# Kernel tuning notes

Measured on AMD Instinct MI355X. Metric: run time of the kernel, lower is better.

## Reference

```python
import jax, jax.numpy as jnp
import numpy as np
import math

B, N, D, H, BS = 1, 2048, 1024, 16, 256  # batch, seq, d_model, heads, block_size


def setup_inputs() -> dict:
    key = jax.random.key(0)
    ks = jax.random.split(key, 8)
    s = 0.02  # init scale for projection weights
    return {
        "x": jax.random.normal(ks[0], (B, N, D), jnp.float32),
        "distance_bias": jax.random.uniform(ks[1], (N, N), dtype=jnp.float32),
        "Wq": jax.random.normal(ks[2], (D, D), jnp.float32) * s,
        "bq": jnp.zeros((D,), jnp.float32),
        "Wk": jax.random.normal(ks[3], (D, D), jnp.float32) * s,
        "bk": jnp.zeros((D,), jnp.float32),
        "Wv": jax.random.normal(ks[4], (D, D), jnp.float32) * s,
        "bv": jnp.zeros((D,), jnp.float32),
        "Wo": jax.random.normal(ks[5], (D, D), jnp.float32) * s,
        "bo": jnp.zeros((D,), jnp.float32),
    }


def reference(x, distance_bias, Wq, bq, Wk, bk, Wv, bv, Wo, bo):
    Bm, Nm, Dm = x.shape
    dk = Dm // H
    scale = 1.0 / math.sqrt(dk)
    nb = Nm // BS  # number of blocks along sequence

    def proj(W, b):
        # torch Linear: x @ W.T + b, then split heads -> [B, H, N, dk]
        return (x @ W.T + b).reshape(Bm, Nm, H, dk).transpose(0, 2, 1, 3)

    Q, K, V = proj(Wq, bq), proj(Wk, bk), proj(Wv, bv)

    # scores with toroidal bias subtracted (matches `scores - bias_block`)
    scores = jnp.einsum('bhqd,bhkd->bhqk', Q, K) * scale - distance_bias[None, None]
    # view as [B, H, n_qblk, BS, n_kblk, BS] and softmax PER (q-block, k-block)
    s6 = scores.reshape(Bm, H, nb, BS, nb, BS)
    w = jax.nn.softmax(s6, axis=-1)  # softmax over keys within each kv block

    Vb = V.reshape(Bm, H, nb, BS, dk)
    # sum over all kv blocks of (per-block softmax) @ V_block
    num = jnp.einsum('bhqsnk,bhnkd->bhqsd', w, Vb)  # [B,H,nb,BS,dk]
    # accumulated normalizer = sum of per-block softmax weights over all kv blocks
    norm = jnp.sum(w, axis=(4, 5))  # [B,H,nb,BS]
    O = num / (norm[..., None] + 1e-8)

    O = O.reshape(Bm, H, Nm, dk).transpose(0, 2, 1, 3).reshape(Bm, Nm, Dm)
    return O @ Wo.T + bo
```

## Files before the change

### kernel.cpp

```cpp
#include <hip/hip_runtime.h>
#include <hip/hip_fp16.h>

typedef _Float16 half8 __attribute__((ext_vector_type(8)));
typedef _Float16 half4v __attribute__((ext_vector_type(4)));
typedef float f32x4 __attribute__((ext_vector_type(4)));

#define NSEQ 2048
#define DMOD 1024
#define NHEAD 16
#define DK 64

#define GLOAD_LDS16(gp, lp) __builtin_amdgcn_global_load_lds(                 \
    (const __attribute__((address_space(1))) void*)(gp),                      \
    (__attribute__((address_space(3))) void*)(lp), 16, 0, 0)

#define WAIT_VM(n) (0xF70 | (n))


__global__ __launch_bounds__(256) void cast_pack(
    const float* __restrict__ x, const float* __restrict__ wq,
    const float* __restrict__ wk, const float* __restrict__ wv,
    const float* __restrict__ wo, _Float16* __restrict__ dst)
{
    const int w = blockIdx.x * 4 + (threadIdx.x >> 6);
    const int ln = threadIdx.x & 63, m = ln & 15, qd = ln >> 4;
    const float* src; _Float16* d; int loc;
    if (w < 4096) { src = x; d = dst; loc = w; }
    else {
        const int w2 = w - 4096, mat = w2 >> 11;
        loc = w2 & 2047;
        src = mat == 0 ? wq : mat == 1 ? wk : mat == 2 ? wv : wo;
        d = dst + 2097152 + mat * 1048576;
    }
    const int st = loc >> 5, kc = loc & 31;
    const float* p = src + (size_t)(st * 16 + m) * 1024 + kc * 32 + qd * 8;
    float4 a = *(const float4*)p, b = *(const float4*)(p + 4);
    half8 h;
    h[0] = (_Float16)a.x; h[1] = (_Float16)a.y; h[2] = (_Float16)a.z; h[3] = (_Float16)a.w;
    h[4] = (_Float16)b.x; h[5] = (_Float16)b.y; h[6] = (_Float16)b.z; h[7] = (_Float16)b.w;
    *(half8*)(d + (size_t)(loc * 64 + ln) * 8) = h;
}

__global__ __launch_bounds__(256) void cvt_bias(
    const float* __restrict__ src, _Float16* __restrict__ dst)
{
    int i = (blockIdx.x * 256 + threadIdx.x) * 4;
    float4 v = *(const float4*)(src + i);
    half4v h;
    h[0] = (_Float16)v.x; h[1] = (_Float16)v.y;
    h[2] = (_Float16)v.z; h[3] = (_Float16)v.w;
    *(half4v*)(dst + i) = h;
}

__global__ __launch_bounds__(256) void combine(
    const _Float16* __restrict__ a, const _Float16* __restrict__ b,
    _Float16* __restrict__ o)
{
    int i = (blockIdx.x * 256 + threadIdx.x) * 8;
    half8 x = *(const half8*)(a + i);
    half8 y = *(const half8*)(b + i);
    half8 r;
#pragma unroll
    for (int j = 0; j < 8; ++j) r[j] = (_Float16)((float)x[j] + (float)y[j]);
    *(half8*)(o + i) = r;
}

template<int BM, int BN, int MODE>
__global__ __launch_bounds__(256) void tgemm(
    const _Float16* __restrict__ A,
    const _Float16* __restrict__ W0, const _Float16* __restrict__ W1,
    const _Float16* __restrict__ W2,
    const float* __restrict__ b0, const float* __restrict__ b1,
    const float* __restrict__ b2,
    _Float16* __restrict__ oQ, _Float16* __restrict__ oK,
    _Float16* __restrict__ oV, float* __restrict__ oF)
{
    constexpr int MT = BM / 32, NT = BN / 32;
    constexpr int NA = BM / 64, NB = BN / 64;
    __shared__ _Float16 sA[3 * BM * 32];
    __shared__ _Float16 sB[3 * BN * 32];
    const int tid = threadIdx.x, wv = tid >> 6, ln = tid & 63;
    const int m = ln & 15, qd = ln >> 4;
    const int row0 = blockIdx.x * BM;

    int sel = 0, colbase;
    const _Float16* W; const float* bias;
    if constexpr (MODE == 0) {
        sel = blockIdx.y >> 3;
        colbase = (blockIdx.y & 7) * BN;
        W = sel == 0 ? W0 : sel == 1 ? W1 : W2;
        bias = sel == 0 ? b0 : sel == 1 ? b1 : b2;
    } else {
        colbase = blockIdx.y * BN;
        W = W0; bias = b0;
    }
    const int wr = wv >> 1, wc = wv & 1;

    f32x4 acc[MT][NT];
#pragma unroll
    for (int i = 0; i < MT; ++i)
#pragma unroll
        for (int j = 0; j < NT; ++j) acc[i][j] = (f32x4){0.f, 0.f, 0.f, 0.f};

    auto stage = [&](int kc, int b) {
        _Float16* dA = sA + b * (BM * 32);
        _Float16* dB = sB + b * (BN * 32);
#pragma unroll
        for (int ra = 0; ra < NA; ++ra) {
            const int st = ra * 4 + wv;
            GLOAD_LDS16(A + ((size_t)((row0 >> 4) + st) * 32 + kc) * 512 + ln * 8,
                        dA + st * 512);
        }
#pragma unroll
        for (int rb = 0; rb < NB; ++rb) {
            const int st = rb * 4 + wv;
            GLOAD_LDS16(W + ((size_t)((colbase >> 4) + st) * 32 + kc) * 512 + ln * 8,
                        dB + st * 512);
        }
    };
    auto step = [&](int b) {
        const _Float16* cA = sA + b * (BM * 32);
        const _Float16* cB = sB + b * (BN * 32);
        half8 af[MT], bf[NT];
#pragma unroll
        for (int i = 0; i < MT; ++i)
            af[i] = *(const half8*)(cA + ((wr * MT + i) * 64 + ln) * 8);
#pragma unroll
        for (int j = 0; j < NT; ++j)
            bf[j] = *(const half8*)(cB + ((wc * NT + j) * 64 + ln) * 8);
#pragma unroll
        for (int i = 0; i < MT; ++i)
#pragma unroll
            for (int j = 0; j < NT; ++j)
                acc[i][j] = __builtin_amdgcn_mfma_f32_16x16x32_f16(af[i], bf[j], acc[i][j], 0, 0, 0);
    };

    stage(0, 0);
    stage(1, 1);
#pragma unroll
    for (int kc = 0; kc < 31; ++kc) {
        __builtin_amdgcn_s_waitcnt(WAIT_VM(NA + NB));
        __builtin_amdgcn_s_barrier();
        if (kc < 30) stage(kc + 2, (kc + 2) % 3);
        step(kc % 3);
    }
    __builtin_amdgcn_s_waitcnt(WAIT_VM(0));
    __builtin_amdgcn_s_barrier();
    step(1);

#pragma unroll
    for (int j = 0; j < NT; ++j) {
        const int col = colbase + wc * (BN / 2) + j * 16 + m;
        const float bv = bias[col];
#pragma unroll
        for (int i = 0; i < MT; ++i) {
            const int crow0 = row0 + wr * (BM / 2) + i * 16 + qd * 4;
            if constexpr (MODE == 1) {
#pragma unroll
                for (int r = 0; r < 4; ++r)
                    oF[(size_t)(crow0 + r) * DMOD + col] = acc[i][j][r] + bv;
            } else {
                const int h = col >> 6, d = col & 63;
                if (sel == 0) {
#pragma unroll
                    for (int r = 0; r < 4; ++r)
                        oQ[h * (NSEQ * DK) + (crow0 + r) * DK + d] =
                            (_Float16)((acc[i][j][r] + bv) * 0.125f);
                } else if (sel == 1) {
#pragma unroll
                    for (int r = 0; r < 4; ++r) {
                        const int n = crow0 + r;
                        oK[(size_t)(((h * 16 + (n >> 7)) * 16
                                     + ((n >> 4) & 7) * 2 + (d >> 5)) * 64
                                    + (n & 15) + 16 * ((d >> 3) & 3)) * 8
                           + (d & 7)] = (_Float16)(acc[i][j][r] + bv);
                    }
                } else {
                    half4v hv;
#pragma unroll
                    for (int r = 0; r < 4; ++r) hv[r] = (_Float16)(acc[i][j][r] + bv);
                    const int n0 = crow0;
                    *(half4v*)(oV + (size_t)(((h * 16 + (n0 >> 7)) * 16
                                              + ((n0 >> 5) & 3) * 4 + ((d >> 4) & 3)) * 64
                                             + (d & 15) + 16 * ((n0 >> 3) & 3)) * 8
                               + (n0 & 7)) = hv;
                }
            }
        }
    }
}

__global__ __launch_bounds__(256, 2) void attn(
    const _Float16* __restrict__ Q, const _Float16* __restrict__ Kt,
    const _Float16* __restrict__ Vt, const _Float16* __restrict__ bias_h,
    _Float16* __restrict__ Op)
{
    __shared__ _Float16 sK[8192];
    __shared__ _Float16 sV[8192];
    __shared__ _Float16 sP[16384];
    const int tid = threadIdx.x, wv = tid >> 6, ln = tid & 63;
    const int m = ln & 15, qd = ln >> 4;
    const int h = blockIdx.x;
    const int q0w = blockIdx.y * 128 + wv * 32;
    const int kvb = blockIdx.z * 8;
    const _Float16* Qh = Q + h * (NSEQ * DK);
    const _Float16* Kh = Kt + h * (NSEQ * DK) + kvb * 8192;
    const _Float16* Vh = Vt + h * (NSEQ * DK) + kvb * 8192;
    const _Float16* brow0 = bias_h + (size_t)(q0w + m) * NSEQ + kvb * 128;
    const _Float16* brow1 = bias_h + (size_t)(q0w + 16 + m) * NSEQ + kvb * 128;

    half8 qf[2][2];
#pragma unroll
    for (int u = 0; u < 2; ++u) {
        qf[u][0] = *(const half8*)(Qh + (q0w + u * 16 + m) * DK + qd * 8);
        qf[u][1] = *(const half8*)(Qh + (q0w + u * 16 + m) * DK + 32 + qd * 8);
    }

    f32x4 oacc[2][4], oU[2][4];
#pragma unroll
    for (int u = 0; u < 2; ++u)
#pragma unroll
        for (int v = 0; v < 4; ++v) {
            oacc[u][v] = (f32x4){0.f, 0.f, 0.f, 0.f};
            oU[u][v]   = (f32x4){0.f, 0.f, 0.f, 0.f};
        }
    float bsum[2] = {0.f, 0.f};

    for (int ls = 0; ls < 8; ++ls) {
        if (ls) __syncthreads();
#pragma unroll
        for (int j = 0; j < 4; ++j) {
            const int f = j * 4 + wv;
            GLOAD_LDS16(Kh + ls * 8192 + f * 512 + ln * 8, sK + f * 512);
            GLOAD_LDS16(Vh + ls * 8192 + f * 512 + ln * 8, sV + f * 512);
        }
        half4v bcur[2][8];
#pragma unroll
        for (int t = 0; t < 8; ++t) {
            bcur[0][t] = *(const half4v*)(brow0 + ls * 128 + t * 16 + qd * 4);
            bcur[1][t] = *(const half4v*)(brow1 + ls * 128 + t * 16 + qd * 4);
        }
        __syncthreads();

#pragma unroll
        for (int t = 0; t < 8; ++t) {
            half8 kf0 = *(const half8*)(sK + ((t * 2 + 0) * 64 + ln) * 8);
            half8 kf1 = *(const half8*)(sK + ((t * 2 + 1) * 64 + ln) * 8);
#pragma unroll
            for (int u = 0; u < 2; ++u) {
                f32x4 s = {0.f, 0.f, 0.f, 0.f};
                s = __builtin_amdgcn_mfma_f32_16x16x32_f16(kf0, qf[u][0], s, 0, 0, 0);
                s = __builtin_amdgcn_mfma_f32_16x16x32_f16(kf1, qf[u][1], s, 0, 0, 0);
                float p0 = __expf(s[0] - (float)bcur[u][t][0]);
                float p1 = __expf(s[1] - (float)bcur[u][t][1]);
                float p2 = __expf(s[2] - (float)bcur[u][t][2]);
                float p3 = __expf(s[3] - (float)bcur[u][t][3]);
                bsum[u] += (p0 + p1) + (p2 + p3);
                half4v ph;
                ph[0] = (_Float16)p0; ph[1] = (_Float16)p1;
                ph[2] = (_Float16)p2; ph[3] = (_Float16)p3;
                *(half4v*)(sP + wv * 4096 + u * 2048 + (t >> 1) * 512
                           + (((t & 1) * 2 + (qd >> 1)) * 16 + m) * 8
                           + (qd & 1) * 4) = ph;
            }
        }

#pragma unroll
        for (int kk = 0; kk < 4; ++kk) {
            half8 pa0 = *(const half8*)(sP + wv * 4096 + kk * 512 + ln * 8);
            half8 pa1 = *(const half8*)(sP + wv * 4096 + 2048 + kk * 512 + ln * 8);
#pragma unroll
            for (int vt = 0; vt < 4; ++vt) {
                half8 vb = *(const half8*)(sV + ((kk * 4 + vt) * 64 + ln) * 8);
                oU[0][vt] = __builtin_amdgcn_mfma_f32_16x16x32_f16(pa0, vb, oU[0][vt], 0, 0, 0);
                oU[1][vt] = __builtin_amdgcn_mfma_f32_16x16x32_f16(pa1, vb, oU[1][vt], 0, 0, 0);
            }
        }

        if (ls & 1) {
#pragma unroll
            for (int u = 0; u < 2; ++u) {
                float s2 = bsum[u];
                s2 += __shfl_xor(s2, 16, 64);
                s2 += __shfl_xor(s2, 32, 64);
                float inv = 1.0f / (8.0f * s2);
                float iv[4];
#pragma unroll
                for (int r = 0; r < 4; ++r) iv[r] = __shfl(inv, qd * 4 + r, 64);
#pragma unroll
                for (int vt = 0; vt < 4; ++vt) {
#pragma unroll
                    for (int r = 0; r < 4; ++r) oacc[u][vt][r] += iv[r] * oU[u][vt][r];
                    oU[u][vt] = (f32x4){0.f, 0.f, 0.f, 0.f};
                }
                bsum[u] = 0.f;
            }
        }
    }

    _Float16* Opz = Op + (size_t)blockIdx.z * 2097152;
#pragma unroll
    for (int u = 0; u < 2; ++u) {
        const int st = (q0w >> 4) + u;
#pragma unroll
        for (int vt = 0; vt < 4; ++vt) {
            const int d = h * 64 + vt * 16 + m;
            _Float16* base = Opz + (size_t)(st * 32 + (d >> 5)) * 512
                             + ((d >> 3) & 3) * 128 + (d & 7);
#pragma unroll
            for (int r = 0; r < 4; ++r)
                base[(qd * 4 + r) * 8] = (_Float16)oacc[u][vt][r];
        }
    }
}

extern "C" void kernel_launch(void* const* d_in, const int* in_sizes, int n_in,
                              void* d_out, int out_size, void* d_ws, size_t ws_size,
                              hipStream_t stream)
{
    const float* x  = (const float*)d_in[0];
    const float* db = (const float*)d_in[1];
    const float* Wq = (const float*)d_in[2];
    const float* bq = (const float*)d_in[3];
    const float* Wk = (const float*)d_in[4];
    const float* bk = (const float*)d_in[5];
    const float* Wv = (const float*)d_in[6];
    const float* bv = (const float*)d_in[7];
    const float* Wo = (const float*)d_in[8];
    const float* bo = (const float*)d_in[9];
    float* out = (float*)d_out;

    _Float16* ws  = (_Float16*)d_ws;
    _Float16* xh  = ws;
    _Float16* wqh = xh  + 2097152;
    _Float16* wkh = wqh + 1048576;
    _Float16* wvh = wkh + 1048576;
    _Float16* woh = wvh + 1048576;
    _Float16* Qb  = woh + 1048576;
    _Float16* Kb  = Qb  + 2097152;
    _Float16* Vtb = Kb  + 2097152;
    _Float16* Oh0 = Vtb + 2097152;
    _Float16* Oh1 = Oh0 + 2097152;
    _Float16* bh  = ws;

    cast_pack<<<3072, 256, 0, stream>>>(x, Wq, Wk, Wv, Wo, xh);

    tgemm<128, 128, 0><<<dim3(16, 24), 256, 0, stream>>>(
        xh, wqh, wkh, wvh, bq, bk, bv, Qb, Kb, Vtb, nullptr);

    cvt_bias<<<4096, 256, 0, stream>>>(db, bh);

    attn<<<dim3(NHEAD, NSEQ / 128, 2), 256, 0, stream>>>(Qb, Kb, Vtb, bh, Oh0);

    combine<<<1024, 256, 0, stream>>>(Oh0, Oh1, Oh0);

    tgemm<64, 128, 1><<<dim3(32, 8), 256, 0, stream>>>(
        Oh0, woh, nullptr, nullptr, bo, nullptr, nullptr,
        nullptr, nullptr, nullptr, out);
}
```

Before: 187.0 us.

## Double-buffer K tiles and prefetch next bias rows in attention loop

The attention kernel now double-buffers K tiles in LDS, issuing the next step's K loads while the current step computes. It also prefetches the next step's bias registers after the QK/softmax phase. Manual s_waitcnt counters and raw s_barrier calls replace __syncthreads, so V loads can keep flying during the score computation. The cost is an extra 16 KB of LDS, which may hurt the 2-blocks-per-CU occupancy. The hand-counted vmcnt values are also fragile and could cause races if they are wrong.

```diff
diff --git a/kernel.cpp b/kernel.cpp
--- a/kernel.cpp
+++ b/kernel.cpp
@@ -15,6 +15,9 @@
     (__attribute__((address_space(3))) void*)(lp), 16, 0, 0)
 
 #define WAIT_VM(n) (0xF70 | (n))
+#define WAIT_VM_BIG(n) ((((n) >> 4) << 14) | 0xF70 | ((n) & 0xF))
+
+template<bool B> struct Bc { static constexpr bool value = B; };
 
 
 __global__ __launch_bounds__(256) void cast_pack(
@@ -195,7 +198,7 @@
     const _Float16* __restrict__ Vt, const _Float16* __restrict__ bias_h,
     _Float16* __restrict__ Op)
 {
-    __shared__ _Float16 sK[8192];
+    __shared__ _Float16 sK[2][8192];
     __shared__ _Float16 sV[8192];
     __shared__ _Float16 sP[16384];
     const int tid = threadIdx.x, wv = tid >> 6, ln = tid & 63;
@@ -216,6 +219,18 @@
         qf[u][1] = *(const half8*)(Qh + (q0w + u * 16 + m) * DK + 32 + qd * 8);
     }
 
+#pragma unroll
+    for (int j = 0; j < 4; ++j) {
+        const int f = j * 4 + wv;
+        GLOAD_LDS16(Kh + f * 512 + ln * 8, sK[0] + f * 512);
+    }
+    half4v bcur[2][8];
+#pragma unroll
+    for (int t = 0; t < 8; ++t) {
+        bcur[0][t] = *(const half4v*)(brow0 + t * 16 + qd * 4);
+        bcur[1][t] = *(const half4v*)(brow1 + t * 16 + qd * 4);
+    }
+
     f32x4 oacc[2][4], oU[2][4];
 #pragma unroll
     for (int u = 0; u < 2; ++u)
@@ -226,26 +241,32 @@
         }
     float bsum[2] = {0.f, 0.f};
 
-    for (int ls = 0; ls < 8; ++ls) {
-        if (ls) __syncthreads();
+    auto do_step = [&](int ls, auto fc, auto lc) {
+        constexpr bool FIRST = decltype(fc)::value;
+        constexpr bool LAST  = decltype(lc)::value;
+        if constexpr (!FIRST) __builtin_amdgcn_s_barrier();
 #pragma unroll
         for (int j = 0; j < 4; ++j) {
             const int f = j * 4 + wv;
-            GLOAD_LDS16(Kh + ls * 8192 + f * 512 + ln * 8, sK + f * 512);
             GLOAD_LDS16(Vh + ls * 8192 + f * 512 + ln * 8, sV + f * 512);
         }
-        half4v bcur[2][8];
+        if constexpr (!LAST) {
+#pragma unroll
+            for (int j = 0; j < 4; ++j) {
+                const int f = j * 4 + wv;
+                GLOAD_LDS16(Kh + (ls + 1) * 8192 + f * 512 + ln * 8,
+                            sK[(ls + 1) & 1] + f * 512);
+            }
+        }
+        if constexpr (LAST) __builtin_amdgcn_s_waitcnt(WAIT_VM(4));
+        else                __builtin_amdgcn_s_waitcnt(WAIT_VM(8));
+        __builtin_amdgcn_s_barrier();
+
+        const _Float16* sKc = sK[ls & 1];
 #pragma unroll
         for (int t = 0; t < 8; ++t) {
-            bcur[0][t] = *(const half4v*)(brow0 + ls * 128 + t * 16 + qd * 4);
-            bcur[1][t] = *(const half4v*)(brow1 + ls * 128 + t * 16 + qd * 4);
-        }
-        __syncthreads();
-
-#pragma unroll
-        for (int t = 0; t < 8; ++t) {
-            half8 kf0 = *(const half8*)(sK + ((t * 2 + 0) * 64 + ln) * 8);
-            half8 kf1 = *(const half8*)(sK + ((t * 2 + 1) * 64 + ln) * 8);
+            half8 kf0 = *(const half8*)(sKc + ((t * 2 + 0) * 64 + ln) * 8);
+            half8 kf1 = *(const half8*)(sKc + ((t * 2 + 1) * 64 + ln) * 8);
 #pragma unroll
             for (int u = 0; u < 2; ++u) {
                 f32x4 s = {0.f, 0.f, 0.f, 0.f};
@@ -265,6 +286,20 @@
             }
         }
 
+        if constexpr (!LAST) {
+            __builtin_amdgcn_sched_barrier(0);
+#pragma unroll
+            for (int t = 0; t < 8; ++t) {
+                bcur[0][t] = *(const half4v*)(brow0 + (ls + 1) * 128 + t * 16 + qd * 4);
+                bcur[1][t] = *(const half4v*)(brow1 + (ls + 1) * 128 + t * 16 + qd * 4);
+            }
+            __builtin_amdgcn_sched_barrier(0);
+        }
+
+        if constexpr (LAST) __builtin_amdgcn_s_waitcnt(WAIT_VM(0));
+        else                __builtin_amdgcn_s_waitcnt(WAIT_VM_BIG(20));
+        __builtin_amdgcn_s_barrier();
+
 #pragma unroll
         for (int kk = 0; kk < 4; ++kk) {
             half8 pa0 = *(const half8*)(sP + wv * 4096 + kk * 512 + ln * 8);
@@ -296,7 +331,11 @@
                 bsum[u] = 0.f;
             }
         }
-    }
+    };
+
+    do_step(0, Bc<true>{}, Bc<false>{});
+    for (int ls = 1; ls < 7; ++ls) do_step(ls, Bc<false>{}, Bc<false>{});
+    do_step(7, Bc<false>{}, Bc<true>{});
 
     _Float16* Opz = Op + (size_t)blockIdx.z * 2097152;
 #pragma unroll
```

Measured after the change: 190.6 us. No clear change (+1.9%).

## Split attention work across 8 waves with 16 query rows each

Applied to the files above, without the earlier changes.

The attention kernel now runs 512 threads per block, so each wave handles 16 query rows instead of 32. The block still covers 128 queries and shares the same K/V tiles in LDS. Each wave loads fewer K/V fragments and keeps half the accumulators, which cuts register pressure and allows more waves per CU (launch bounds 512,4). The cost is that each K/V fragment read from LDS is now reused over fewer query rows, so LDS traffic per MFMA roughly doubles.

```diff
diff --git a/kernel.cpp b/kernel.cpp
--- a/kernel.cpp
+++ b/kernel.cpp
@@ -190,7 +190,7 @@
     }
 }
 
-__global__ __launch_bounds__(256, 2) void attn(
+__global__ __launch_bounds__(512, 4) void attn(
     const _Float16* __restrict__ Q, const _Float16* __restrict__ Kt,
     const _Float16* __restrict__ Vt, const _Float16* __restrict__ bias_h,
     _Float16* __restrict__ Op)
@@ -201,116 +201,95 @@
     const int tid = threadIdx.x, wv = tid >> 6, ln = tid & 63;
     const int m = ln & 15, qd = ln >> 4;
     const int h = blockIdx.x;
-    const int q0w = blockIdx.y * 128 + wv * 32;
+    const int q0 = blockIdx.y * 128 + wv * 16;
     const int kvb = blockIdx.z * 8;
     const _Float16* Qh = Q + h * (NSEQ * DK);
     const _Float16* Kh = Kt + h * (NSEQ * DK) + kvb * 8192;
     const _Float16* Vh = Vt + h * (NSEQ * DK) + kvb * 8192;
-    const _Float16* brow0 = bias_h + (size_t)(q0w + m) * NSEQ + kvb * 128;
-    const _Float16* brow1 = bias_h + (size_t)(q0w + 16 + m) * NSEQ + kvb * 128;
-
-    half8 qf[2][2];
-#pragma unroll
-    for (int u = 0; u < 2; ++u) {
-        qf[u][0] = *(const half8*)(Qh + (q0w + u * 16 + m) * DK + qd * 8);
-        qf[u][1] = *(const half8*)(Qh + (q0w + u * 16 + m) * DK + 32 + qd * 8);
-    }
-
-    f32x4 oacc[2][4], oU[2][4];
-#pragma unroll
-    for (int u = 0; u < 2; ++u)
-#pragma unroll
-        for (int v = 0; v < 4; ++v) {
-            oacc[u][v] = (f32x4){0.f, 0.f, 0.f, 0.f};
-            oU[u][v]   = (f32x4){0.f, 0.f, 0.f, 0.f};
-        }
-    float bsum[2] = {0.f, 0.f};
+    const _Float16* brow = bias_h + (size_t)(q0 + m) * NSEQ + kvb * 128;
+
+    half8 qf[2];
+    qf[0] = *(const half8*)(Qh + (q0 + m) * DK + qd * 8);
+    qf[1] = *(const half8*)(Qh + (q0 + m) * DK + 32 + qd * 8);
+
+    f32x4 oacc[4], oU[4];
+#pragma unroll
+    for (int v = 0; v < 4; ++v) {
+        oacc[v] = (f32x4){0.f, 0.f, 0.f, 0.f};
+        oU[v]   = (f32x4){0.f, 0.f, 0.f, 0.f};
+    }
+    float bsum = 0.f;
 
     for (int ls = 0; ls < 8; ++ls) {
         if (ls) __syncthreads();
-#pragma unroll
-        for (int j = 0; j < 4; ++j) {
-            const int f = j * 4 + wv;
-            GLOAD_LDS16(Kh + ls * 8192 + f * 512 + ln * 8, sK + f * 512);
-            GLOAD_LDS16(Vh + ls * 8192 + f * 512 + ln * 8, sV + f * 512);
-        }
-        half4v bcur[2][8];
-#pragma unroll
-        for (int t = 0; t < 8; ++t) {
-            bcur[0][t] = *(const half4v*)(brow0 + ls * 128 + t * 16 + qd * 4);
-            bcur[1][t] = *(const half4v*)(brow1 + ls * 128 + t * 16 + qd * 4);
-        }
+        GLOAD_LDS16(Kh + ls * 8192 + wv * 512 + ln * 8, sK + wv * 512);
+        GLOAD_LDS16(Kh + ls * 8192 + (wv + 8) * 512 + ln * 8, sK + (wv + 8) * 512);
+        GLOAD_LDS16(Vh + ls * 8192 + wv * 512 + ln * 8, sV + wv * 512);
+        GLOAD_LDS16(Vh + ls * 8192 + (wv + 8) * 512 + ln * 8, sV + (wv + 8) * 512);
+        half4v bcur[8];
+#pragma unroll
+        for (int t = 0; t < 8; ++t)
+            bcur[t] = *(const half4v*)(brow + ls * 128 + t * 16 + qd * 4);
         __syncthreads();
 
 #pragma unroll
         for (int t = 0; t < 8; ++t) {
             half8 kf0 = *(const half8*)(sK + ((t * 2 + 0) * 64 + ln) * 8);
             half8 kf1 = *(const half8*)(sK + ((t * 2 + 1) * 64 + ln) * 8);
-#pragma unroll
-            for (int u = 0; u < 2; ++u) {
-                f32x4 s = {0.f, 0.f, 0.f, 0.f};
-                s = __builtin_amdgcn_mfma_f32_16x16x32_f16(kf0, qf[u][0], s, 0, 0, 0);
-                s = __builtin_amdgcn_mfma_f32_16x16x32_f16(kf1, qf[u][1], s, 0, 0, 0);
-                float p0 = __expf(s[0] - (float)bcur[u][t][0]);
-                float p1 = __expf(s[1] - (float)bcur[u][t][1]);
-                float p2 = __expf(s[2] - (float)bcur[u][t][2]);
-                float p3 = __expf(s[3] - (float)bcur[u][t][3]);
-                bsum[u] += (p0 + p1) + (p2 + p3);
-                half4v ph;
-                ph[0] = (_Float16)p0; ph[1] = (_Float16)p1;
-                ph[2] = (_Float16)p2; ph[3] = (_Float16)p3;
-                *(half4v*)(sP + wv * 4096 + u * 2048 + (t >> 1) * 512
-                           + (((t & 1) * 2 + (qd >> 1)) * 16 + m) * 8
-                           + (qd & 1) * 4) = ph;
-            }
+            f32x4 s = {0.f, 0.f, 0.f, 0.f};
+            s = __builtin_amdgcn_mfma_f32_16x16x32_f16(kf0, qf[0], s, 0, 0, 0);
+            s = __builtin_amdgcn_mfma_f32_16x16x32_f16(kf1, qf[1], s, 0, 0, 0);
+            float p0 = __expf(s[0] - (float)bcur[t][0]);
+            float p1 = __expf(s[1] - (float)bcur[t][1]);
+            float p2 = __expf(s[2] - (float)bcur[t][2]);
+            float p3 = __expf(s[3] - (float)bcur[t][3]);
+            bsum += (p0 + p1) + (p2 + p3);
+            half4v ph;
+            ph[0] = (_Float16)p0; ph[1] = (_Float16)p1;
+            ph[2] = (_Float16)p2; ph[3] = (_Float16)p3;
+            *(half4v*)(sP + wv * 2048 + (t >> 1) * 512
+                       + (((t & 1) * 2 + (qd >> 1)) * 16 + m) * 8
+                       + (qd & 1) * 4) = ph;
         }
 
 #pragma unroll
         for (int kk = 0; kk < 4; ++kk) {
-            half8 pa0 = *(const half8*)(sP + wv * 4096 + kk * 512 + ln * 8);
-            half8 pa1 = *(const half8*)(sP + wv * 4096 + 2048 + kk * 512 + ln * 8);
+            half8 pa = *(const half8*)(sP + wv * 2048 + kk * 512 + ln * 8);
 #pragma unroll
             for (int vt = 0; vt < 4; ++vt) {
                 half8 vb = *(const half8*)(sV + ((kk * 4 + vt) * 64 + ln) * 8);
-                oU[0][vt] = __builtin_amdgcn_mfma_f32_16x16x32_f16(pa0, vb, oU[0][vt], 0, 0, 0);
-                oU[1][vt] = __builtin_amdgcn_mfma_f32_16x16x32_f16(pa1, vb, oU[1][vt], 0, 0, 0);
+                oU[vt] = __builtin_amdgcn_mfma_f32_16x16x32_f16(pa, vb, oU[vt], 0, 0, 0);
             }
         }
 
         if (ls & 1) {
-#pragma unroll
-            for (int u = 0; u < 2; ++u) {
-                float s2 = bsum[u];
-                s2 += __shfl_xor(s2, 16, 64);
-                s2 += __shfl_xor(s2, 32, 64);
-                float inv = 1.0f / (8.0f * s2);
-                float iv[4];
-#pragma unroll
-                for (int r = 0; r < 4; ++r) iv[r] = __shfl(inv, qd * 4 + r, 64);
-#pragma unroll
-                for (int vt = 0; vt < 4; ++vt) {
-#pragma unroll
-                    for (int r = 0; r < 4; ++r) oacc[u][vt][r] += iv[r] * oU[u][vt][r];
-                    oU[u][vt] = (f32x4){0.f, 0.f, 0.f, 0.f};
-                }
-                bsum[u] = 0.f;
+            float s2 = bsum;
+            s2 += __shfl_xor(s2, 16, 64);
+            s2 += __shfl_xor(s2, 32, 64);
+            float inv = 1.0f / (8.0f * s2);
+            float iv[4];
+#pragma unroll
+            for (int r = 0; r < 4; ++r) iv[r] = __shfl(inv, qd * 4 + r, 64);
+#pragma unroll
+            for (int vt = 0; vt < 4; ++vt) {
+#pragma unroll
+                for (int r = 0; r < 4; ++r) oacc[vt][r] += iv[r] * oU[vt][r];
+                oU[vt] = (f32x4){0.f, 0.f, 0.f, 0.f};
             }
+            bsum = 0.f;
         }
     }
 
     _Float16* Opz = Op + (size_t)blockIdx.z * 2097152;
-#pragma unroll
-    for (int u = 0; u < 2; ++u) {
-        const int st = (q0w >> 4) + u;
-#pragma unroll
-        for (int vt = 0; vt < 4; ++vt) {
-            const int d = h * 64 + vt * 16 + m;
-            _Float16* base = Opz + (size_t)(st * 32 + (d >> 5)) * 512
-                             + ((d >> 3) & 3) * 128 + (d & 7);
-#pragma unroll
-            for (int r = 0; r < 4; ++r)
-                base[(qd * 4 + r) * 8] = (_Float16)oacc[u][vt][r];
-        }
+    const int st = blockIdx.y * 8 + wv;
+#pragma unroll
+    for (int vt = 0; vt < 4; ++vt) {
+        const int d = h * 64 + vt * 16 + m;
+        _Float16* base = Opz + (size_t)(st * 32 + (d >> 5)) * 512
+                         + ((d >> 3) & 3) * 128 + (d & 7);
+#pragma unroll
+        for (int r = 0; r < 4; ++r)
+            base[(qd * 4 + r) * 8] = (_Float16)oacc[vt][r];
     }
 }
 
@@ -350,7 +329,7 @@
 
     cvt_bias<<<4096, 256, 0, stream>>>(db, bh);
 
-    attn<<<dim3(NHEAD, NSEQ / 128, 2), 256, 0, stream>>>(Qb, Kb, Vtb, bh, Oh0);
+    attn<<<dim3(NHEAD, NSEQ / 128, 2), 512, 0, stream>>>(Qb, Kb, Vtb, bh, Oh0);
 
     combine<<<1024, 256, 0, stream>>>(Oh0, Oh1, Oh0);
 
```

Measured after the change: 185.3 us. No clear change (-0.9%).
